# Kernel optimization log

Measured on AMD Instinct MI355X. Metric: run time of the kernel, lower is better.

The kernel has to match this reference:

```python
import jax, jax.numpy as jnp
import numpy as np

B, S, D, H = 2, 2048, 1024, 16
HD = D // H
SCALE = float(np.sqrt(HD))


def setup_inputs() -> dict:
    key = jax.random.key(0)
    ks = jax.random.split(key, 11)
    std = 1.0 / np.sqrt(D)
    inp = {
        "query": jax.random.normal(ks[0], (B, S, D), dtype=jnp.float32),
        "key": jax.random.normal(ks[1], (B, S, D), dtype=jnp.float32),
        "value": jax.random.normal(ks[2], (B, S, D), dtype=jnp.float32),
        "w_q": jax.random.normal(ks[3], (D, D), dtype=jnp.float32) * std,
        "b_q": jax.random.normal(ks[4], (D,), dtype=jnp.float32) * std,
        "w_k": jax.random.normal(ks[5], (D, D), dtype=jnp.float32) * std,
        "b_k": jax.random.normal(ks[6], (D,), dtype=jnp.float32) * std,
        "w_v": jax.random.normal(ks[7], (D, D), dtype=jnp.float32) * std,
        "b_v": jax.random.normal(ks[8], (D,), dtype=jnp.float32) * std,
        "w_fc": jax.random.normal(ks[9], (D, D), dtype=jnp.float32) * std,
        "b_fc": jax.random.normal(ks[10], (D,), dtype=jnp.float32) * std,
    }
    return inp


def reference(query, key, value, w_q, b_q, w_k, b_k, w_v, b_v, w_fc, b_fc):
    # Linear projections (torch Linear: x @ W^T + b; here w_* stored as [in, out])
    Q = query @ w_q + b_q            # [B, S, D]
    K = key @ w_k + b_k
    V = value @ w_v + b_v
    # split heads -> [B, H, S, HD]
    Q = Q.reshape(B, S, H, HD).transpose(0, 2, 1, 3)
    K = K.reshape(B, S, H, HD).transpose(0, 2, 1, 3)
    V = V.reshape(B, S, H, HD).transpose(0, 2, 1, 3)
    energy = jnp.einsum('bhqd,bhkd->bhqk', Q, K) / SCALE  # [B, H, S, S]
    attn = jax.nn.softmax(energy, axis=-1)
    x = jnp.einsum('bhqk,bhkd->bhqd', attn, V)            # [B, H, S, HD]
    x = x.transpose(0, 2, 1, 3).reshape(B, S, D)
    return x @ w_fc + b_fc
```

## Files before the change

kernel.cpp:

```cpp
#include <hip/hip_runtime.h>
#include <stdint.h>

#define Bz 2
#define Sz 2048
#define Dz 1024
#define Hz 16
#define HDz 64
#define Mz (Bz*Sz)

typedef unsigned short u16;
typedef __attribute__((ext_vector_type(8))) __bf16 bf16x8;
typedef __attribute__((ext_vector_type(8))) unsigned short u16x8;
typedef __attribute__((ext_vector_type(4))) float f32x4;

#define C1 0.1803368801111243f

__device__ __forceinline__ u16 f2bf(float f) {
  union { float f; unsigned u; } v; v.f = f;
  unsigned r = v.u + 0x7fffu + ((v.u >> 16) & 1u);
  return (u16)(r >> 16);
}

__device__ __forceinline__ unsigned packbf(float a, float b) {
  unsigned ua = __builtin_bit_cast(unsigned, a);
  unsigned ub = __builtin_bit_cast(unsigned, b);
  return ((ua + 0x8000u) >> 16) | ((ub + 0x8000u) & 0xFFFF0000u);
}

__device__ __forceinline__ bf16x8 mk8(unsigned a, unsigned b, unsigned c, unsigned d) {
  union { unsigned u[4]; bf16x8 v; } x;
  x.u[0] = a; x.u[1] = b; x.u[2] = c; x.u[3] = d;
  return x.v;
}

__device__ __forceinline__ void async16(void* lds, const void* g) {
  __builtin_amdgcn_global_load_lds(
      (const __attribute__((address_space(1))) unsigned int*)g,
      (__attribute__((address_space(3))) unsigned int*)lds, 16, 0, 0);
}

__global__ void __launch_bounds__(256)
prep_kernel(const float* __restrict__ q, const float* __restrict__ k, const float* __restrict__ v,
            const float* __restrict__ w0, const float* __restrict__ w1,
            const float* __restrict__ w2, const float* __restrict__ w3,
            u16* __restrict__ xq, u16* __restrict__ xk, u16* __restrict__ xv,
            u16* __restrict__ Wt) {
  __shared__ __align__(16) float t[32][33];
  const int bid = blockIdx.x, tid = threadIdx.x;
  if (bid < 12288) {
    const int sel = bid >> 12;
    const int i = ((bid & 4095) << 8) + tid;
    const float* in = sel == 0 ? q : sel == 1 ? k : v;
    u16* out = sel == 0 ? xq : sel == 1 ? xk : xv;
    float4 tv = ((const float4*)in)[i];
    ((ushort4*)out)[i] = make_ushort4(f2bf(tv.x), f2bf(tv.y), f2bf(tv.z), f2bf(tv.w));
  } else {
    const int idx = bid - 12288;
    const int z = idx >> 10, r = idx & 1023;
    const int n0 = (r & 31) * 32, k0 = (r >> 5) * 32;
    const float* W = z == 0 ? w0 : z == 1 ? w1 : z == 2 ? w2 : w3;
    u16* o = Wt + (size_t)z * Dz * Dz;
    const int x = tid & 31, y = tid >> 5;
#pragma unroll
    for (int i = 0; i < 4; ++i)
      t[y + i*8][x] = W[(size_t)(k0 + y + i*8) * Dz + n0 + x];
    __syncthreads();
#pragma unroll
    for (int i = 0; i < 4; ++i)
      o[(size_t)(n0 + y + i*8) * Dz + k0 + x] = f2bf(t[x][y + i*8]);
  }
}

__global__ void __launch_bounds__(256)
vtrans_kernel(const u16* __restrict__ Vp, u16* __restrict__ Vt) {
  __shared__ __align__(16) u16 t[64][72];
  int s0 = blockIdx.x * 64, bh = blockIdx.y;
  int b = bh >> 4;
  int h = bh & 15;
  int tid = threadIdx.x;
#pragma unroll
  for (int p = 0; p < 4; ++p) {
    int c = p * 256 + tid;
    int row = c >> 4, off = (c & 15) * 4;
    ushort4 v = *(const ushort4*)(Vp + (size_t)(b * Sz + s0 + row) * Dz + h * 64 + off);
    *(ushort4*)&t[row][off] = v;
  }
  __syncthreads();
#pragma unroll
  for (int p = 0; p < 4; ++p) {
    int c = p * 256 + tid;
    int d = c >> 4, sc = (c & 15) * 4;
    ushort4 v = make_ushort4(t[sc + 0][d], t[sc + 1][d], t[sc + 2][d], t[sc + 3][d]);
    *(ushort4*)(Vt + (size_t)(bh * 64 + d) * Sz + s0 + sc) = v;
  }
}

__global__ void __launch_bounds__(256)
gemm_qkv(const u16* __restrict__ xq, const u16* __restrict__ xk, const u16* __restrict__ xv,
         const u16* __restrict__ Wt3,
         const float* __restrict__ bq, const float* __restrict__ bk, const float* __restrict__ bv,
         u16* __restrict__ Qp, u16* __restrict__ Kp, u16* __restrict__ Vp)
{
  __shared__ __align__(16) u16 lA[128][32];
  __shared__ __align__(16) u16 lB[128][32];
  const int sel = blockIdx.x >> 3;
  const int n0 = (blockIdx.x & 7) * 128;
  const int m0 = blockIdx.y * 128;
  const u16* A = sel == 0 ? xq : sel == 1 ? xk : xv;
  const u16* Bt = Wt3 + (size_t)sel * Dz * Dz;
  const float* bias = sel == 0 ? bq : sel == 1 ? bk : bv;
  u16* Cv = sel == 0 ? Qp : sel == 1 ? Kp : Vp;

  const int tid = threadIdx.x;
  const int w = tid >> 6, lane = tid & 63;
  const int wm = (w >> 1) * 64, wn = (w & 1) * 64;
  const int l16 = lane & 15, qd = lane >> 4;

  f32x4 acc[4][4];
#pragma unroll
  for (int i = 0; i < 4; ++i)
#pragma unroll
    for (int j = 0; j < 4; ++j) acc[i][j] = (f32x4){0.f, 0.f, 0.f, 0.f};

  const int r0 = tid >> 2, c0 = (tid & 3) * 8;
  const int r1 = r0 + 64;

  for (int k0 = 0; k0 < Dz; k0 += 32) {
    __syncthreads();
    async16(&lA[r0][c0], A  + (size_t)(m0 + r0) * Dz + k0 + c0);
    async16(&lB[r0][c0], Bt + (size_t)(n0 + r0) * Dz + k0 + c0);
    async16(&lA[r1][c0], A  + (size_t)(m0 + r1) * Dz + k0 + c0);
    async16(&lB[r1][c0], Bt + (size_t)(n0 + r1) * Dz + k0 + c0);
    __syncthreads();
    bf16x8 af[4], bfv[4];
#pragma unroll
    for (int t = 0; t < 4; ++t) {
      af[t]  = *(const bf16x8*)&lA[wm + t * 16 + l16][qd * 8];
      bfv[t] = *(const bf16x8*)&lB[wn + t * 16 + l16][qd * 8];
    }
#pragma unroll
    for (int mt = 0; mt < 4; ++mt)
#pragma unroll
      for (int nt = 0; nt < 4; ++nt)
        acc[mt][nt] = __builtin_amdgcn_mfma_f32_16x16x32_bf16(af[mt], bfv[nt], acc[mt][nt], 0, 0, 0);
  }

#pragma unroll
  for (int nt = 0; nt < 4; ++nt) {
    const int n = n0 + wn + nt * 16 + l16;
    const float bvl = bias[n];
#pragma unroll
    for (int mt = 0; mt < 4; ++mt)
#pragma unroll
      for (int r = 0; r < 4; ++r) {
        const int m = m0 + wm + mt * 16 + qd * 4 + r;
        Cv[(size_t)m * Dz + n] = f2bf(acc[mt][nt][r] + bvl);
      }
  }
}

__global__ void __launch_bounds__(256)
gemm_fc(const u16* __restrict__ A, const u16* __restrict__ Bt,
        const float* __restrict__ bias, float* __restrict__ C)
{
  __shared__ __align__(16) u16 lA[128][32];
  __shared__ __align__(16) u16 lB[64][32];
  const int m0 = blockIdx.y * 128, n0 = blockIdx.x * 64;
  const int tid = threadIdx.x;
  const int w = tid >> 6, lane = tid & 63;
  const int wm = (w >> 1) * 64, wn = (w & 1) * 32;
  const int l16 = lane & 15, qd = lane >> 4;

  f32x4 acc[4][2];
#pragma unroll
  for (int i = 0; i < 4; ++i)
#pragma unroll
    for (int j = 0; j < 2; ++j) acc[i][j] = (f32x4){0.f, 0.f, 0.f, 0.f};

  const int r0 = tid >> 2, c0 = (tid & 3) * 8;

  for (int k0 = 0; k0 < Dz; k0 += 32) {
    __syncthreads();
    async16(&lA[r0][c0],      A  + (size_t)(m0 + r0) * Dz + k0 + c0);
    async16(&lA[r0 + 64][c0], A  + (size_t)(m0 + r0 + 64) * Dz + k0 + c0);
    async16(&lB[r0][c0],      Bt + (size_t)(n0 + r0) * Dz + k0 + c0);
    __syncthreads();
    bf16x8 af[4], bfv[2];
#pragma unroll
    for (int t = 0; t < 4; ++t)
      af[t] = *(const bf16x8*)&lA[wm + t * 16 + l16][qd * 8];
#pragma unroll
    for (int t = 0; t < 2; ++t)
      bfv[t] = *(const bf16x8*)&lB[wn + t * 16 + l16][qd * 8];
#pragma unroll
    for (int mt = 0; mt < 4; ++mt)
#pragma unroll
      for (int nt = 0; nt < 2; ++nt)
        acc[mt][nt] = __builtin_amdgcn_mfma_f32_16x16x32_bf16(af[mt], bfv[nt], acc[mt][nt], 0, 0, 0);
  }

#pragma unroll
  for (int nt = 0; nt < 2; ++nt) {
    const int n = n0 + wn + nt * 16 + l16;
    const float bvl = bias[n];
#pragma unroll
    for (int mt = 0; mt < 4; ++mt)
#pragma unroll
      for (int r = 0; r < 4; ++r) {
        const int m = m0 + wm + mt * 16 + qd * 4 + r;
        C[(size_t)m * Dz + n] = acc[mt][nt][r] + bvl;
      }
  }
}

__global__ void __launch_bounds__(256, 3)
attn_kernel(const u16* __restrict__ Qp, const u16* __restrict__ Kp,
            const u16* __restrict__ Vt, u16* __restrict__ Ao)
{
  __shared__ __align__(16) u16 lK[128][72];
  __shared__ __align__(16) u16 lV[64][136];

  const int q0 = blockIdx.x * 128;
  const int bh = blockIdx.y;
  const int b = bh >> 4, h = bh & 15;
  const int tid = threadIdx.x, w = tid >> 6, lane = tid & 63;
  const int l16 = lane & 15, qd = lane >> 4;

  const int krow = tid >> 3, kcol = (tid & 7) * 8;
  const int vrow = tid >> 4, vcol = (tid & 15) * 8;

  u16x8 kreg[4], vreg[4];
#pragma unroll
  for (int p = 0; p < 4; ++p) {
    kreg[p] = *(const u16x8*)(Kp + (size_t)(b * Sz + p * 32 + krow) * Dz + h * 64 + kcol);
    vreg[p] = *(const u16x8*)(Vt + (size_t)(bh * 64 + p * 16 + vrow) * Sz + vcol);
  }

  bf16x8 qf[2][2];
#pragma unroll
  for (int qt = 0; qt < 2; ++qt)
#pragma unroll
    for (int ksd = 0; ksd < 2; ++ksd)
      qf[qt][ksd] = *(const bf16x8*)(Qp + (size_t)(b * Sz + q0 + w * 32 + qt * 16 + l16) * Dz
                                     + h * 64 + ksd * 32 + qd * 8);

  u16x8 ob;
#pragma unroll
  for (int i = 0; i < 8; ++i) ob[i] = 0x3F80u;
  const bf16x8 onesA = __builtin_bit_cast(bf16x8, ob);

  const int sidx0 = ((qd & 1) * 2) * 16 + l16;

  f32x4 oaccT[4][2];
  f32x4 laccT[2];
#pragma unroll
  for (int mt = 0; mt < 4; ++mt)
#pragma unroll
    for (int qt = 0; qt < 2; ++qt) oaccT[mt][qt] = (f32x4){0.f, 0.f, 0.f, 0.f};
  laccT[0] = (f32x4){0.f, 0.f, 0.f, 0.f};
  laccT[1] = (f32x4){0.f, 0.f, 0.f, 0.f};

  for (int t = 0; t < Sz / 128; ++t) {
    __syncthreads();
#pragma unroll
    for (int p = 0; p < 4; ++p) {
      *(u16x8*)&lK[p * 32 + krow][kcol] = kreg[p];
      *(u16x8*)&lV[p * 16 + vrow][vcol] = vreg[p];
    }
    if (t + 1 < Sz / 128) {
      const int kv = (t + 1) * 128;
#pragma unroll
      for (int p = 0; p < 4; ++p) {
        kreg[p] = *(const u16x8*)(Kp + (size_t)(b * Sz + kv + p * 32 + krow) * Dz + h * 64 + kcol);
        vreg[p] = *(const u16x8*)(Vt + (size_t)(bh * 64 + p * 16 + vrow) * Sz + kv + vcol);
      }
    }
    __syncthreads();

    f32x4 st[8][2];
#pragma unroll
    for (int i = 0; i < 8; ++i)
#pragma unroll
      for (int j = 0; j < 2; ++j) st[i][j] = (f32x4){0.f, 0.f, 0.f, 0.f};
#pragma unroll
    for (int ksd = 0; ksd < 2; ++ksd) {
      bf16x8 kf[8];
#pragma unroll
      for (int kvt = 0; kvt < 8; ++kvt)
        kf[kvt] = *(const bf16x8*)&lK[kvt * 16 + l16][ksd * 32 + qd * 8];
#pragma unroll
      for (int kvt = 0; kvt < 8; ++kvt)
#pragma unroll
        for (int qt = 0; qt < 2; ++qt)
          st[kvt][qt] = __builtin_amdgcn_mfma_f32_16x16x32_bf16(kf[kvt], qf[qt][ksd], st[kvt][qt], 0, 0, 0);
    }

#pragma unroll
    for (int ks = 0; ks < 4; ++ks) {
      unsigned pkl[2][2][2];
#pragma unroll
      for (int j = 0; j < 2; ++j)
#pragma unroll
        for (int qt = 0; qt < 2; ++qt) {
          const f32x4 s4 = st[2 * ks + j][qt];
          float e0 = exp2f(s4[0] * C1);
          float e1 = exp2f(s4[1] * C1);
          float e2 = exp2f(s4[2] * C1);
          float e3 = exp2f(s4[3] * C1);
          pkl[j][qt][0] = packbf(e0, e1);
          pkl[j][qt][1] = packbf(e2, e3);
        }

      bf16x8 vfA[4];
#pragma unroll
      for (int mt = 0; mt < 4; ++mt)
        vfA[mt] = *(const bf16x8*)&lV[mt * 16 + l16][ks * 32 + qd * 8];

#pragma unroll
      for (int qt = 0; qt < 2; ++qt) {
        unsigned v[4];
#pragma unroll
        for (int i = 0; i < 4; ++i) {
          const int si = sidx0 + (i >> 1) * 16;
          unsigned tA = (unsigned)__shfl((int)pkl[0][qt][i & 1], si);
          unsigned tB = (unsigned)__shfl((int)pkl[1][qt][i & 1], si);
          v[i] = (qd & 2) ? tB : tA;
        }
        const bf16x8 pb = mk8(v[0], v[1], v[2], v[3]);
#pragma unroll
        for (int mt = 0; mt < 4; ++mt)
          oaccT[mt][qt] = __builtin_amdgcn_mfma_f32_16x16x32_bf16(vfA[mt], pb, oaccT[mt][qt], 0, 0, 0);
        laccT[qt] = __builtin_amdgcn_mfma_f32_16x16x32_bf16(onesA, pb, laccT[qt], 0, 0, 0);
      }
    }
  }

  float inv[2];
  inv[0] = 1.0f / laccT[0][0];
  inv[1] = 1.0f / laccT[1][0];
#pragma unroll
  for (int mt = 0; mt < 4; ++mt)
#pragma unroll
    for (int qt = 0; qt < 2; ++qt) {
      const int q = b * Sz + q0 + w * 32 + qt * 16 + l16;
      ushort4 o = make_ushort4(f2bf(oaccT[mt][qt][0] * inv[qt]),
                               f2bf(oaccT[mt][qt][1] * inv[qt]),
                               f2bf(oaccT[mt][qt][2] * inv[qt]),
                               f2bf(oaccT[mt][qt][3] * inv[qt]));
      *(ushort4*)(Ao + (size_t)q * Dz + h * 64 + mt * 16 + qd * 4) = o;
    }
}

extern "C" void kernel_launch(void* const* d_in, const int* in_sizes, int n_in,
                              void* d_out, int out_size, void* d_ws, size_t ws_size,
                              hipStream_t stream) {
  const float* query = (const float*)d_in[0];
  const float* key   = (const float*)d_in[1];
  const float* value = (const float*)d_in[2];
  const float* w_q  = (const float*)d_in[3];
  const float* b_q  = (const float*)d_in[4];
  const float* w_k  = (const float*)d_in[5];
  const float* b_k  = (const float*)d_in[6];
  const float* w_v  = (const float*)d_in[7];
  const float* b_v  = (const float*)d_in[8];
  const float* w_fc = (const float*)d_in[9];
  const float* b_fc = (const float*)d_in[10];
  float* out = (float*)d_out;

  const size_t XE = (size_t)Mz * Dz;
  const size_t WE = (size_t)Dz * Dz;
  u16* Xq  = (u16*)d_ws;
  u16* Xk  = Xq + XE;
  u16* Xv  = Xk + XE;
  u16* Wt  = Xv + XE;
  u16* Wtf = Wt + 3 * WE;
  u16* Qp  = Wt + 4 * WE;
  u16* Kp  = Qp + XE;
  u16* Vp  = Kp + XE;
  u16* Vt  = Xk;
  u16* Ao  = Xq;

  prep_kernel<<<16384, 256, 0, stream>>>(query, key, value, w_q, w_k, w_v, w_fc,
                                         Xq, Xk, Xv, Wt);

  gemm_qkv<<<dim3(24, Mz / 128), 256, 0, stream>>>(Xq, Xk, Xv, Wt, b_q, b_k, b_v, Qp, Kp, Vp);

  vtrans_kernel<<<dim3(Sz / 64, Bz * Hz), 256, 0, stream>>>(Vp, Vt);

  attn_kernel<<<dim3(Sz / 128, Bz * Hz), 256, 0, stream>>>(Qp, Kp, Vt, Ao);

  gemm_fc<<<dim3(Dz / 64, Mz / 128), 256, 0, stream>>>(Ao, Wtf, b_fc, out);
}
```

Baseline: 299.6 us.

## Interleave QK^T per slice and compute softmax row sums with VALU adds

The QK^T score computation is moved inside the per-32-column PV loop, so only a 2x2 block of score accumulators is live at a time instead of the full 8x2. This cuts register pressure and lets the exp/PV work overlap with the next slice's MFMAs. The softmax denominator is no longer produced by an extra MFMA against a ones matrix. Each lane now keeps an fp32 running sum of its exponentials, reduced across lanes with shuffles at the end. That removes two MFMAs per slice, but the sum now uses unrounded values while the numerator still uses bf16-rounded ones.

```diff
diff --git a/kernel.cpp b/kernel.cpp
--- a/kernel.cpp
+++ b/kernel.cpp
@@ -244,21 +244,14 @@
       qf[qt][ksd] = *(const bf16x8*)(Qp + (size_t)(b * Sz + q0 + w * 32 + qt * 16 + l16) * Dz
                                      + h * 64 + ksd * 32 + qd * 8);
 
-  u16x8 ob;
-#pragma unroll
-  for (int i = 0; i < 8; ++i) ob[i] = 0x3F80u;
-  const bf16x8 onesA = __builtin_bit_cast(bf16x8, ob);
-
   const int sidx0 = ((qd & 1) * 2) * 16 + l16;
 
   f32x4 oaccT[4][2];
-  f32x4 laccT[2];
 #pragma unroll
   for (int mt = 0; mt < 4; ++mt)
 #pragma unroll
     for (int qt = 0; qt < 2; ++qt) oaccT[mt][qt] = (f32x4){0.f, 0.f, 0.f, 0.f};
-  laccT[0] = (f32x4){0.f, 0.f, 0.f, 0.f};
-  laccT[1] = (f32x4){0.f, 0.f, 0.f, 0.f};
+  float lsum[2] = {0.f, 0.f};
 
   for (int t = 0; t < Sz / 128; ++t) {
     __syncthreads();
@@ -277,36 +270,34 @@
     }
     __syncthreads();
 
-    f32x4 st[8][2];
-#pragma unroll
-    for (int i = 0; i < 8; ++i)
-#pragma unroll
-      for (int j = 0; j < 2; ++j) st[i][j] = (f32x4){0.f, 0.f, 0.f, 0.f};
-#pragma unroll
-    for (int ksd = 0; ksd < 2; ++ksd) {
-      bf16x8 kf[8];
-#pragma unroll
-      for (int kvt = 0; kvt < 8; ++kvt)
-        kf[kvt] = *(const bf16x8*)&lK[kvt * 16 + l16][ksd * 32 + qd * 8];
-#pragma unroll
-      for (int kvt = 0; kvt < 8; ++kvt)
-#pragma unroll
-        for (int qt = 0; qt < 2; ++qt)
-          st[kvt][qt] = __builtin_amdgcn_mfma_f32_16x16x32_bf16(kf[kvt], qf[qt][ksd], st[kvt][qt], 0, 0, 0);
-    }
-
 #pragma unroll
     for (int ks = 0; ks < 4; ++ks) {
+      f32x4 st[2][2];
+#pragma unroll
+      for (int j = 0; j < 2; ++j)
+#pragma unroll
+        for (int qt = 0; qt < 2; ++qt) st[j][qt] = (f32x4){0.f, 0.f, 0.f, 0.f};
+#pragma unroll
+      for (int ksd = 0; ksd < 2; ++ksd) {
+        bf16x8 kf0 = *(const bf16x8*)&lK[(2 * ks    ) * 16 + l16][ksd * 32 + qd * 8];
+        bf16x8 kf1 = *(const bf16x8*)&lK[(2 * ks + 1) * 16 + l16][ksd * 32 + qd * 8];
+#pragma unroll
+        for (int qt = 0; qt < 2; ++qt) {
+          st[0][qt] = __builtin_amdgcn_mfma_f32_16x16x32_bf16(kf0, qf[qt][ksd], st[0][qt], 0, 0, 0);
+          st[1][qt] = __builtin_amdgcn_mfma_f32_16x16x32_bf16(kf1, qf[qt][ksd], st[1][qt], 0, 0, 0);
+        }
+      }
+
       unsigned pkl[2][2][2];
 #pragma unroll
       for (int j = 0; j < 2; ++j)
 #pragma unroll
         for (int qt = 0; qt < 2; ++qt) {
-          const f32x4 s4 = st[2 * ks + j][qt];
-          float e0 = exp2f(s4[0] * C1);
-          float e1 = exp2f(s4[1] * C1);
-          float e2 = exp2f(s4[2] * C1);
-          float e3 = exp2f(s4[3] * C1);
+          float e0 = exp2f(st[j][qt][0] * C1);
+          float e1 = exp2f(st[j][qt][1] * C1);
+          float e2 = exp2f(st[j][qt][2] * C1);
+          float e3 = exp2f(st[j][qt][3] * C1);
+          lsum[qt] += (e0 + e1) + (e2 + e3);
           pkl[j][qt][0] = packbf(e0, e1);
           pkl[j][qt][1] = packbf(e2, e3);
         }
@@ -330,14 +321,19 @@
 #pragma unroll
         for (int mt = 0; mt < 4; ++mt)
           oaccT[mt][qt] = __builtin_amdgcn_mfma_f32_16x16x32_bf16(vfA[mt], pb, oaccT[mt][qt], 0, 0, 0);
-        laccT[qt] = __builtin_amdgcn_mfma_f32_16x16x32_bf16(onesA, pb, laccT[qt], 0, 0, 0);
       }
     }
   }
 
   float inv[2];
-  inv[0] = 1.0f / laccT[0][0];
-  inv[1] = 1.0f / laccT[1][0];
+#pragma unroll
+  for (int qt = 0; qt < 2; ++qt) {
+    float lq = lsum[qt];
+    lq += __shfl_xor(lq, 16);
+    lq += __shfl_xor(lq, 32);
+    inv[qt] = 1.0f / lq;
+  }
+
 #pragma unroll
   for (int mt = 0; mt < 4; ++mt)
 #pragma unroll
```

After: 276.5 us. -7.7%, faster.
